# Optimization experiments

Measured on AMD Instinct MI355X. Metric: run time of the kernel, lower is better.

## Reference

```python
import jax, jax.numpy as jnp
import numpy as np

B, C, T = 8, 256, 16000
N_HALF = 32  # d_state // 2 complex modes (S4D stores conjugate pairs)
EPS = 1e-8


def setup_inputs() -> dict:
    key = jax.random.key(0)
    ks = jax.random.split(key, 8)
    x = jax.random.normal(ks[0], (B, C, T), jnp.float32)
    # ChannelwiseLayerNorm params
    gamma = jnp.ones((C,), jnp.float32)
    beta = jnp.zeros((C,), jnp.float32)
    # PReLU per-channel slope (torch default init 0.25)
    prelu_w = jnp.full((C,), 0.25, jnp.float32)
    # S4D kernel params (standard S4D init)
    log_dt = (jax.random.uniform(ks[1], (C,), jnp.float32)
              * (np.log(0.1) - np.log(0.001)) + np.log(0.001)).astype(jnp.float32)
    log_A_real = jnp.log(0.5 * jnp.ones((C, N_HALF), jnp.float32))
    A_imag = jnp.broadcast_to(np.pi * jnp.arange(N_HALF, dtype=jnp.float32), (C, N_HALF))
    C_re = jax.random.normal(ks[2], (C, N_HALF), jnp.float32) * (0.5 ** 0.5)
    C_im = jax.random.normal(ks[3], (C, N_HALF), jnp.float32) * (0.5 ** 0.5)
    D = jax.random.normal(ks[4], (C,), jnp.float32)
    # output 1x1 conv (C -> 2C) followed by GLU over channel dim
    W_out = jax.random.normal(ks[5], (2 * C, C), jnp.float32) * (1.0 / np.sqrt(C))
    b_out = jnp.zeros((2 * C,), jnp.float32)
    return dict(x=x, gamma=gamma, beta=beta, prelu_w=prelu_w, log_dt=log_dt,
                log_A_real=log_A_real, A_imag=A_imag, C_re=C_re, C_im=C_im,
                D=D, W_out=W_out, b_out=b_out)


def reference(x, gamma, beta, prelu_w, log_dt, log_A_real, A_imag, C_re, C_im, D, W_out, b_out):
    # --- channel-wise LayerNorm over C (per timestep), x: [B, C, T] ---
    mean = jnp.mean(x, axis=1, keepdims=True)
    var = jnp.mean((x - mean) ** 2, axis=1, keepdims=True)
    y = (x - mean) * jax.lax.rsqrt(var + EPS)
    y = y * gamma[None, :, None] + beta[None, :, None]
    # --- PReLU (per-channel slope) ---
    y = jnp.where(y >= 0, y, prelu_w[None, :, None] * y)
    # --- S4D convolution kernel via Vandermonde (ZOH discretization) ---
    L = x.shape[-1]
    dt = jnp.exp(log_dt)[:, None]                      # [C, 1]
    A = -jnp.exp(log_A_real) + 1j * A_imag             # [C, N]
    dtA = dt * A                                       # [C, N]
    Cc = (C_re + 1j * C_im) * (jnp.exp(dtA) - 1.0) / A  # [C, N]
    vand = jnp.exp(dtA[:, :, None] * jnp.arange(L))    # [C, N, L]
    k = 2.0 * jnp.real(jnp.einsum('hn,hnl->hl', Cc, vand))  # [C, L]
    # --- FFT-based causal convolution ---
    n = 2 * L
    y_f = jnp.fft.rfft(y, n=n)                         # [B, C, n/2+1]
    k_f = jnp.fft.rfft(k, n=n)                         # [C, n/2+1]
    s = jnp.fft.irfft(y_f * k_f[None], n=n)[..., :L]   # [B, C, T]
    s = s + y * D[None, :, None]                       # skip connection
    # --- GELU + 1x1 conv + GLU over channels ---
    s = jax.nn.gelu(s, approximate=False)
    z = jnp.einsum('bct,oc->bot', s, W_out) + b_out[None, :, None]  # [B, 2C, T]
    out = z[:, :C] * jax.nn.sigmoid(z[:, C:])
    # --- residual ---
    return x + out
```

## Files before the change

kernel.cpp:

```cpp
#include <hip/hip_runtime.h>
#include <cstdint>
#include <cstddef>

constexpr int cB = 8, cC = 256, cT = 16000, cN = 32;
constexpr int cLAM = 128;
constexpr int cP = 125;
constexpr int cPpad = 128;
constexpr float cEPS = 1e-8f;

typedef __bf16 bf16;
typedef __bf16 bf16x4 __attribute__((ext_vector_type(4)));
typedef __bf16 bf16x8 __attribute__((ext_vector_type(8)));
typedef float floatx4 __attribute__((ext_vector_type(4)));

constexpr size_t kMean = 0;
constexpr size_t kRstd = kMean + (size_t)cB * cT * 4;
constexpr size_t kWlr  = kRstd + (size_t)cB * cT * 4;
constexpr size_t kWli  = kWlr + (size_t)cC * cN * 4;
constexpr size_t kWb   = kWli + (size_t)cC * cN * 4;
constexpr size_t kLt   = kWb  + (size_t)512 * 256 * 2;
constexpr size_t kEt   = kLt  + (size_t)cC * 128 * 128 * 2;
constexpr size_t kVt   = kEt  + (size_t)cC * 64 * 128 * 2;
constexpr size_t kU    = kVt  + (size_t)cC * 128 * 64 * 2;

__global__ void prepW_kernel(const float* __restrict__ W_out, bf16* __restrict__ Wb) {
  int idx = blockIdx.x * 256 + threadIdx.x;
  if (idx < 512 * 256) Wb[idx] = (bf16)W_out[idx];
}

__global__ void prep2_kernel(const float* __restrict__ log_dt,
                             const float* __restrict__ log_A_real,
                             const float* __restrict__ A_imag,
                             const float* __restrict__ C_re,
                             const float* __restrict__ C_im,
                             float* __restrict__ wlr, float* __restrict__ wli,
                             bf16* __restrict__ Lt, bf16* __restrict__ Et,
                             bf16* __restrict__ Vt) {
  int c = blockIdx.x;
  int j = threadIdx.x;
  __shared__ float kv[128];
  float dt = expf(log_dt[c]);
  float kj = 0.f;
  for (int n = 0; n < cN; ++n) {
    int idx = c * cN + n;
    float Ar = -expf(log_A_real[idx]);
    float Ai = A_imag[idx];
    float ar = dt * Ar, ai = dt * Ai;
    float mg = expf(ar), cw, sw;
    sincosf(ai, &sw, &cw);
    float wre = mg * cw, wim = mg * sw;
    float den = Ar * Ar + Ai * Ai;
    float emr = wre - 1.f, emi = wim;
    float qr = (emr * Ar + emi * Ai) / den;
    float qi = (emi * Ar - emr * Ai) / den;
    float cre = C_re[idx], cim = C_im[idx];
    float c2r = 2.f * (cre * qr - cim * qi);
    float c2i = 2.f * (cre * qi + cim * qr);
    float mj = expf((float)j * ar), cj, sj;
    sincosf((float)j * ai, &sj, &cj);
    float wjr = mj * cj, wji = mj * sj;
    kj += c2r * wjr - c2i * wji;
    float w1r = wjr * wre - wji * wim;
    float w1i = wjr * wim + wji * wre;
    Vt[(size_t)c * 8192 + j * 64 + 2 * n]     = (bf16)(c2r * w1r - c2i * w1i);
    Vt[(size_t)c * 8192 + j * 64 + 2 * n + 1] = (bf16)(-(c2r * w1i + c2i * w1r));
    float mr = expf((float)(127 - j) * ar), cr2, sr2;
    sincosf((float)(127 - j) * ai, &sr2, &cr2);
    Et[(size_t)c * 8192 + (2 * n) * 128 + j]     = (bf16)(mr * cr2);
    Et[(size_t)c * 8192 + (2 * n + 1) * 128 + j] = (bf16)(mr * sr2);
  }
  kv[j] = kj;
  if (j < cN) {
    int idx = c * cN + j;
    float Ar = -expf(log_A_real[idx]);
    float ai = dt * A_imag[idx], ar = dt * Ar;
    float m = expf(128.f * ar), cc, ss;
    sincosf(128.f * ai, &ss, &cc);
    wlr[idx] = m * cc;
    wli[idx] = m * ss;
  }
  __syncthreads();
  bf16* row = Lt + (size_t)c * 16384 + (size_t)j * 128;
  for (int i = 0; i < 128; i += 4) {
    bf16x4 v;
    for (int q = 0; q < 4; ++q) {
      int ii = i + q;
      v[q] = (ii <= j) ? (bf16)kv[j - ii] : (bf16)0.f;
    }
    *(bf16x4*)(row + i) = v;
  }
}

__global__ void stats_kernel(const float* __restrict__ x,
                             float* __restrict__ meanp, float* __restrict__ rstdp) {
  int g = blockIdx.x * 256 + threadIdx.x;
  int b = g / cT;
  int t = g - b * cT;
  const float* xp = x + (size_t)b * cC * cT + t;
  float s1 = 0.f, s2 = 0.f;
#pragma unroll 8
  for (int c = 0; c < cC; ++c) {
    float v = xp[(size_t)c * cT];
    s1 += v;
    s2 = fmaf(v, v, s2);
  }
  float mean = s1 * (1.0f / cC);
  float var = fmaf(s2, 1.0f / cC, -mean * mean);
  meanp[g] = mean;
  rstdp[g] = rsqrtf(var + cEPS);
}

__global__ __launch_bounds__(256, 2)
void scanM_kernel(const float* __restrict__ x, const float* __restrict__ meanp,
                  const float* __restrict__ rstdp, const float* __restrict__ gam,
                  const float* __restrict__ bet, const float* __restrict__ prw,
                  const float* __restrict__ Dp,
                  const float* __restrict__ wlr, const float* __restrict__ wli,
                  const bf16* __restrict__ Lt, const bf16* __restrict__ Et,
                  const bf16* __restrict__ Vt, bf16* __restrict__ U) {
  __shared__ __align__(16) bf16 Y[128 * 136];
  __shared__ __align__(16) bf16 H[128 * 136];
  __shared__ float Sseg[8][32][2];

  int blk = blockIdx.x;
  int b = blk & 7, c = blk >> 3;
  int tid = threadIdx.x;
  int lane = tid & 63, w = tid >> 6, quad = lane >> 4, mh = lane & 15;
  float gamma = gam[c], beta = bet[c], pw = prw[c], Dc = Dp[c];

  const float4* x4 = (const float4*)(x + (size_t)(b * cC + c) * cT);
  const float4* m4 = (const float4*)(meanp + (size_t)b * cT);
  const float4* r4 = (const float4*)(rstdp + (size_t)b * cT);
#pragma unroll
  for (int it = 0; it < 16; ++it) {
    int i4 = tid + it * 256;
    if (i4 < 4000) {
      float4 xv = x4[i4], mv = m4[i4], rv = r4[i4];
      int t = i4 * 4, p = t >> 7, j = t & 127;
      float ys[4];
      ys[0] = fmaf((xv.x - mv.x) * rv.x, gamma, beta);
      ys[1] = fmaf((xv.y - mv.y) * rv.y, gamma, beta);
      ys[2] = fmaf((xv.z - mv.z) * rv.z, gamma, beta);
      ys[3] = fmaf((xv.w - mv.w) * rv.w, gamma, beta);
      bf16x4 yv;
#pragma unroll
      for (int q = 0; q < 4; ++q) {
        float y = ys[q];
        yv[q] = (bf16)(y >= 0.f ? y : y * pw);
      }
      *(bf16x4*)&Y[p * 136 + j] = yv;
    }
  }
  for (int e = tid; e < 3 * 136; e += 256) Y[125 * 136 + e] = (bf16)0.f;
  __syncthreads();

  const bf16* EtC = Et + (size_t)c * 8192;
  floatx4 hacc[8];
#pragma unroll
  for (int mi = 0; mi < 8; ++mi) hacc[mi] = (floatx4){0.f, 0.f, 0.f, 0.f};
#pragma unroll
  for (int kk = 0; kk < 4; ++kk) {
    bf16x8 bfrag = *(const bf16x8*)(EtC + (w * 16 + mh) * 128 + kk * 32 + quad * 8);
#pragma unroll
    for (int mi = 0; mi < 8; ++mi) {
      bf16x8 af = *(bf16x8*)&Y[(mi * 16 + mh) * 136 + kk * 32 + quad * 8];
      hacc[mi] = __builtin_amdgcn_mfma_f32_16x16x32_bf16(af, bfrag, hacc[mi], 0, 0, 0);
    }
  }
#pragma unroll
  for (int mi = 0; mi < 8; ++mi) {
#pragma unroll
    for (int r = 0; r < 4; ++r) {
      int p = mi * 16 + quad * 4 + r;
      int comp = w * 16 + mh;
      float v = hacc[mi][r];
      bf16 hi = (bf16)v;
      bf16 lo = (bf16)(v - (float)hi);
      H[p * 136 + comp] = hi;
      H[p * 136 + 64 + comp] = lo;
    }
  }
  __syncthreads();

  {
    int n = tid & 31, sg = tid >> 5;
    int p0 = sg * 16;
    int p1 = (p0 + 16 < cP) ? p0 + 16 : cP;
    float wr = wlr[c * cN + n], wi = wli[c * cN + n];
    float hR = 0.f, hI = 0.f;
    for (int p = p0; p < p1; ++p) {
      float sr = (float)H[p * 136 + 2 * n] + (float)H[p * 136 + 64 + 2 * n];
      float si = (float)H[p * 136 + 2 * n + 1] + (float)H[p * 136 + 64 + 2 * n + 1];
      float t1 = fmaf(wr, hR, fmaf(-wi, hI, sr));
      hI = fmaf(wr, hI, fmaf(wi, hR, si));
      hR = t1;
    }
    Sseg[sg][n][0] = hR; Sseg[sg][n][1] = hI;
    __syncthreads();
    if (tid < 32) {
      float ar = wr, ai = wi;
      for (int q = 0; q < 4; ++q) {
        float nr = ar * ar - ai * ai;
        ai = 2.f * ar * ai; ar = nr;
      }
      float HR = 0.f, HI = 0.f;
      for (int s2 = 0; s2 < 8; ++s2) {
        float fr = Sseg[s2][n][0], fi = Sseg[s2][n][1];
        Sseg[s2][n][0] = HR; Sseg[s2][n][1] = HI;
        float t1 = fmaf(ar, HR, fmaf(-ai, HI, fr));
        HI = fmaf(ar, HI, fmaf(ai, HR, fi));
        HR = t1;
      }
    }
    __syncthreads();
    hR = Sseg[sg][n][0]; hI = Sseg[sg][n][1];
    for (int p = p0; p < p1; ++p) {
      float sr = (float)H[p * 136 + 2 * n] + (float)H[p * 136 + 64 + 2 * n];
      float si = (float)H[p * 136 + 2 * n + 1] + (float)H[p * 136 + 64 + 2 * n + 1];
      bf16 hiR = (bf16)hR; bf16 loR = (bf16)(hR - (float)hiR);
      bf16 hiI = (bf16)hI; bf16 loI = (bf16)(hI - (float)hiI);
      H[p * 136 + 2 * n] = hiR;      H[p * 136 + 2 * n + 1] = hiI;
      H[p * 136 + 64 + 2 * n] = loR; H[p * 136 + 64 + 2 * n + 1] = loI;
      float t1 = fmaf(wr, hR, fmaf(-wi, hI, sr));
      hI = fmaf(wr, hI, fmaf(wi, hR, si));
      hR = t1;
    }
  }
  __syncthreads();

  const bf16* LtC = Lt + (size_t)c * 16384;
  const bf16* VtC = Vt + (size_t)c * 8192;
  floatx4 acc[8][2];
#pragma unroll
  for (int mi = 0; mi < 8; ++mi) {
    acc[mi][0] = (floatx4){0.f, 0.f, 0.f, 0.f};
    acc[mi][1] = (floatx4){0.f, 0.f, 0.f, 0.f};
  }
#pragma unroll
  for (int kk = 0; kk < 4; ++kk) {
    bf16x8 b0 = *(const bf16x8*)(LtC + ((2 * w) * 16 + mh) * 128 + kk * 32 + quad * 8);
    bf16x8 b1 = *(const bf16x8*)(LtC + ((2 * w + 1) * 16 + mh) * 128 + kk * 32 + quad * 8);
#pragma unroll
    for (int mi = 0; mi < 8; ++mi) {
      bf16x8 af = *(bf16x8*)&Y[(mi * 16 + mh) * 136 + kk * 32 + quad * 8];
      acc[mi][0] = __builtin_amdgcn_mfma_f32_16x16x32_bf16(af, b0, acc[mi][0], 0, 0, 0);
      acc[mi][1] = __builtin_amdgcn_mfma_f32_16x16x32_bf16(af, b1, acc[mi][1], 0, 0, 0);
    }
  }
#pragma unroll
  for (int kk = 0; kk < 2; ++kk) {
    bf16x8 v0 = *(const bf16x8*)(VtC + ((2 * w) * 16 + mh) * 64 + kk * 32 + quad * 8);
    bf16x8 v1 = *(const bf16x8*)(VtC + ((2 * w + 1) * 16 + mh) * 64 + kk * 32 + quad * 8);
#pragma unroll
    for (int mi = 0; mi < 8; ++mi) {
      bf16x8 ah = *(bf16x8*)&H[(mi * 16 + mh) * 136 + kk * 32 + quad * 8];
      bf16x8 al = *(bf16x8*)&H[(mi * 16 + mh) * 136 + 64 + kk * 32 + quad * 8];
      acc[mi][0] = __builtin_amdgcn_mfma_f32_16x16x32_bf16(ah, v0, acc[mi][0], 0, 0, 0);
      acc[mi][1] = __builtin_amdgcn_mfma_f32_16x16x32_bf16(ah, v1, acc[mi][1], 0, 0, 0);
      acc[mi][0] = __builtin_amdgcn_mfma_f32_16x16x32_bf16(al, v0, acc[mi][0], 0, 0, 0);
      acc[mi][1] = __builtin_amdgcn_mfma_f32_16x16x32_bf16(al, v1, acc[mi][1], 0, 0, 0);
    }
  }
  bf16 ub[8][2][4];
#pragma unroll
  for (int mi = 0; mi < 8; ++mi)
#pragma unroll
    for (int jj = 0; jj < 2; ++jj)
#pragma unroll
      for (int r = 0; r < 4; ++r) {
        int p = mi * 16 + quad * 4 + r;
        int j = (2 * w + jj) * 16 + mh;
        float y = (float)Y[p * 136 + j];
        float sv = fmaf(Dc, y, acc[mi][jj][r]);
        float g = 0.5f * sv * (1.0f + erff(sv * 0.70710678118654752f));
        ub[mi][jj][r] = (bf16)g;
      }
  __syncthreads();
#pragma unroll
  for (int mi = 0; mi < 8; ++mi)
#pragma unroll
    for (int jj = 0; jj < 2; ++jj)
#pragma unroll
      for (int r = 0; r < 4; ++r) {
        int p = mi * 16 + quad * 4 + r;
        int j = (2 * w + jj) * 16 + mh;
        Y[p * 136 + j] = ub[mi][jj][r];
      }
  __syncthreads();
  bf16* Uc = U + (size_t)(b * cC + c) * cT;
#pragma unroll
  for (int it = 0; it < 16; ++it) {
    int i4 = tid + it * 256;
    if (i4 < 4000) {
      int t = i4 * 4, p = t >> 7, j = t & 127;
      *(bf16x4*)(Uc + t) = *(bf16x4*)&Y[p * 136 + j];
    }
  }
}

__global__ __launch_bounds__(256, 2)
void gemm2_kernel(const bf16* __restrict__ U, const bf16* __restrict__ Wb,
                  const float* __restrict__ b_out, const float* __restrict__ x,
                  float* __restrict__ out) {
  __shared__ __align__(16) bf16 Ut[64 * 264];
  int bx = blockIdx.x;
  int tb = bx % 250, b = bx / 250;
  int t0 = tb * 64;
  int tid = threadIdx.x, lane = tid & 63, w = tid >> 6, quad = lane >> 4, mh = lane & 15;
  {
    const bf16* src = U + (size_t)(b * cC + tid) * cT + t0;
#pragma unroll
    for (int g = 0; g < 8; ++g) {
      bf16x8 v = *(const bf16x8*)(src + g * 8);
#pragma unroll
      for (int k = 0; k < 8; ++k) Ut[(g * 8 + k) * 264 + tid] = v[k];
    }
  }
  __syncthreads();
  floatx4 a1[4][4], a2[4][4];
#pragma unroll
  for (int oj = 0; oj < 4; ++oj)
#pragma unroll
    for (int tt = 0; tt < 4; ++tt) {
      a1[oj][tt] = (floatx4){0.f, 0.f, 0.f, 0.f};
      a2[oj][tt] = (floatx4){0.f, 0.f, 0.f, 0.f};
    }
#pragma unroll
  for (int kk = 0; kk < 8; ++kk) {
    int ko = kk * 32 + quad * 8;
    bf16x8 wf1[4], wf2[4];
#pragma unroll
    for (int oj = 0; oj < 4; ++oj) {
      int o = w * 64 + oj * 16 + mh;
      wf1[oj] = *(const bf16x8*)(Wb + (size_t)o * 256 + ko);
      wf2[oj] = *(const bf16x8*)(Wb + (size_t)(o + 256) * 256 + ko);
    }
#pragma unroll
    for (int tt = 0; tt < 4; ++tt) {
      bf16x8 uf = *(bf16x8*)&Ut[(tt * 16 + mh) * 264 + ko];
#pragma unroll
      for (int oj = 0; oj < 4; ++oj) {
        a1[oj][tt] = __builtin_amdgcn_mfma_f32_16x16x32_bf16(wf1[oj], uf, a1[oj][tt], 0, 0, 0);
        a2[oj][tt] = __builtin_amdgcn_mfma_f32_16x16x32_bf16(wf2[oj], uf, a2[oj][tt], 0, 0, 0);
      }
    }
  }
#pragma unroll
  for (int oj = 0; oj < 4; ++oj)
#pragma unroll
    for (int tt = 0; tt < 4; ++tt)
#pragma unroll
      for (int r = 0; r < 4; ++r) {
        int o = w * 64 + oj * 16 + quad * 4 + r;
        int t = t0 + tt * 16 + mh;
        float z1 = a1[oj][tt][r] + b_out[o];
        float z2 = a2[oj][tt][r] + b_out[o + 256];
        float sg = 1.0f / (1.0f + expf(-z2));
        size_t idx = (size_t)(b * cC + o) * cT + t;
        out[idx] = x[idx] + z1 * sg;
      }
}

extern "C" void kernel_launch(void* const* d_in, const int* in_sizes, int n_in,
                              void* d_out, int out_size, void* d_ws, size_t ws_size,
                              hipStream_t stream) {
  const float* x          = (const float*)d_in[0];
  const float* gamma      = (const float*)d_in[1];
  const float* beta       = (const float*)d_in[2];
  const float* prelu_w    = (const float*)d_in[3];
  const float* log_dt     = (const float*)d_in[4];
  const float* log_A_real = (const float*)d_in[5];
  const float* A_imag     = (const float*)d_in[6];
  const float* C_re       = (const float*)d_in[7];
  const float* C_im       = (const float*)d_in[8];
  const float* Dp         = (const float*)d_in[9];
  const float* W_out      = (const float*)d_in[10];
  const float* b_out      = (const float*)d_in[11];
  float* out = (float*)d_out;
  char* ws = (char*)d_ws;

  float* meanp = (float*)(ws + kMean);
  float* rstdp = (float*)(ws + kRstd);
  float* wlr   = (float*)(ws + kWlr);
  float* wli   = (float*)(ws + kWli);
  bf16*  Wb    = (bf16*)(ws + kWb);
  bf16*  Lt    = (bf16*)(ws + kLt);
  bf16*  Et    = (bf16*)(ws + kEt);
  bf16*  Vt    = (bf16*)(ws + kVt);
  bf16*  U     = (bf16*)(ws + kU);

  prepW_kernel<<<512, 256, 0, stream>>>(W_out, Wb);
  prep2_kernel<<<256, 128, 0, stream>>>(log_dt, log_A_real, A_imag, C_re, C_im,
                                        wlr, wli, Lt, Et, Vt);
  stats_kernel<<<(cB * cT) / 256, 256, 0, stream>>>(x, meanp, rstdp);
  scanM_kernel<<<cB * cC, 256, 0, stream>>>(x, meanp, rstdp, gamma, beta, prelu_w,
                                            Dp, wlr, wli, Lt, Et, Vt, U);
  gemm2_kernel<<<cB * (cT / 64), 256, 0, stream>>>(U, Wb, b_out, x, out);
}
```

Baseline: 500.1 us.

## Parallelize stats reduction, split gemm2 outputs, use fast GELU and sigmoid

Restructures the LayerNorm stats kernel so 8 warps each reduce 32 channels and combine through shared memory, which raises parallelism. gemm2 is split into two output-channel halves per time tile with higher occupancy bounds. The exact erf GELU is replaced with the tanh approximation via exp2/rcp intrinsics, and the sigmoid uses fast intrinsics. The Lt Toeplitz write loop is reordered for coalesced stores. The GELU approximation changes numerics slightly, and the gemm2 split reloads the U tile twice.

```diff
diff --git a/kernel.cpp b/kernel.cpp
--- a/kernel.cpp
+++ b/kernel.cpp
@@ -3,9 +3,7 @@
 #include <cstddef>
 
 constexpr int cB = 8, cC = 256, cT = 16000, cN = 32;
-constexpr int cLAM = 128;
 constexpr int cP = 125;
-constexpr int cPpad = 128;
 constexpr float cEPS = 1e-8f;
 
 typedef __bf16 bf16;
@@ -22,6 +20,10 @@
 constexpr size_t kEt   = kLt  + (size_t)cC * 128 * 128 * 2;
 constexpr size_t kVt   = kEt  + (size_t)cC * 64 * 128 * 2;
 constexpr size_t kU    = kVt  + (size_t)cC * 128 * 64 * 2;
+
+__device__ __forceinline__ float fast_sigmoid(float z) {
+  return __builtin_amdgcn_rcpf(1.f + __builtin_amdgcn_exp2f(-z * 1.4426950408889634f));
+}
 
 __global__ void prepW_kernel(const float* __restrict__ W_out, bf16* __restrict__ Wb) {
   int idx = blockIdx.x * 256 + threadIdx.x;
@@ -80,34 +82,48 @@
     wli[idx] = m * ss;
   }
   __syncthreads();
-  bf16* row = Lt + (size_t)c * 16384 + (size_t)j * 128;
-  for (int i = 0; i < 128; i += 4) {
+  bf16* LtC = Lt + (size_t)c * 16384;
+  for (int e = j; e < 4096; e += 128) {
+    int t4 = e * 4;
+    int row = t4 >> 7, col = t4 & 127;
     bf16x4 v;
+#pragma unroll
     for (int q = 0; q < 4; ++q) {
-      int ii = i + q;
-      v[q] = (ii <= j) ? (bf16)kv[j - ii] : (bf16)0.f;
-    }
-    *(bf16x4*)(row + i) = v;
-  }
-}
-
-__global__ void stats_kernel(const float* __restrict__ x,
-                             float* __restrict__ meanp, float* __restrict__ rstdp) {
-  int g = blockIdx.x * 256 + threadIdx.x;
-  int b = g / cT;
-  int t = g - b * cT;
-  const float* xp = x + (size_t)b * cC * cT + t;
+      int ii = col + q;
+      v[q] = (ii <= row) ? (bf16)kv[row - ii] : (bf16)0.f;
+    }
+    *(bf16x4*)(LtC + row * 128 + col) = v;
+  }
+}
+
+__global__ __launch_bounds__(512)
+void stats_kernel(const float* __restrict__ x,
+                  float* __restrict__ meanp, float* __restrict__ rstdp) {
+  __shared__ float r1[8][64], r2[8][64];
+  int g0 = blockIdx.x * 64;
+  int b = g0 / cT;
+  int t0 = g0 - b * cT;
+  int ts = threadIdx.x & 63, cq = threadIdx.x >> 6;
+  const float* xp = x + ((size_t)b * cC + cq * 32) * cT + t0 + ts;
   float s1 = 0.f, s2 = 0.f;
 #pragma unroll 8
-  for (int c = 0; c < cC; ++c) {
+  for (int c = 0; c < 32; ++c) {
     float v = xp[(size_t)c * cT];
     s1 += v;
     s2 = fmaf(v, v, s2);
   }
-  float mean = s1 * (1.0f / cC);
-  float var = fmaf(s2, 1.0f / cC, -mean * mean);
-  meanp[g] = mean;
-  rstdp[g] = rsqrtf(var + cEPS);
+  r1[cq][ts] = s1; r2[cq][ts] = s2;
+  __syncthreads();
+  if (threadIdx.x < 64) {
+    float a1 = 0.f, a2 = 0.f;
+#pragma unroll
+    for (int q = 0; q < 8; ++q) { a1 += r1[q][threadIdx.x]; a2 += r2[q][threadIdx.x]; }
+    float mean = a1 * (1.0f / cC);
+    float var = fmaf(a2, 1.0f / cC, -mean * mean);
+    int g = g0 + threadIdx.x;
+    meanp[g] = mean;
+    rstdp[g] = rsqrtf(var + cEPS);
+  }
 }
 
 __global__ __launch_bounds__(256, 2)
@@ -272,7 +288,11 @@
         int j = (2 * w + jj) * 16 + mh;
         float y = (float)Y[p * 136 + j];
         float sv = fmaf(Dc, y, acc[mi][jj][r]);
-        float g = 0.5f * sv * (1.0f + erff(sv * 0.70710678118654752f));
+        float s3 = sv * sv * sv;
+        float zz = 0.7978845608028654f * fmaf(0.044715f, s3, sv);
+        float e = __builtin_amdgcn_exp2f(zz * 2.8853900817779268f);
+        float th = 1.f - 2.f * __builtin_amdgcn_rcpf(e + 1.f);
+        float g = 0.5f * sv * (1.f + th);
         ub[mi][jj][r] = (bf16)g;
       }
   __syncthreads();
@@ -298,14 +318,17 @@
   }
 }
 
-__global__ __launch_bounds__(256, 2)
+__global__ __launch_bounds__(256, 4)
 void gemm2_kernel(const bf16* __restrict__ U, const bf16* __restrict__ Wb,
                   const float* __restrict__ b_out, const float* __restrict__ x,
                   float* __restrict__ out) {
   __shared__ __align__(16) bf16 Ut[64 * 264];
   int bx = blockIdx.x;
-  int tb = bx % 250, b = bx / 250;
+  int ot = bx & 1;
+  int bt = bx >> 1;
+  int tb = bt % 250, b = bt / 250;
   int t0 = tb * 64;
+  int o0 = ot * 128;
   int tid = threadIdx.x, lane = tid & 63, w = tid >> 6, quad = lane >> 4, mh = lane & 15;
   {
     const bf16* src = U + (size_t)(b * cC + tid) * cT + t0;
@@ -317,9 +340,9 @@
     }
   }
   __syncthreads();
-  floatx4 a1[4][4], a2[4][4];
-#pragma unroll
-  for (int oj = 0; oj < 4; ++oj)
+  floatx4 a1[2][4], a2[2][4];
+#pragma unroll
+  for (int oj = 0; oj < 2; ++oj)
 #pragma unroll
     for (int tt = 0; tt < 4; ++tt) {
       a1[oj][tt] = (floatx4){0.f, 0.f, 0.f, 0.f};
@@ -328,10 +351,10 @@
 #pragma unroll
   for (int kk = 0; kk < 8; ++kk) {
     int ko = kk * 32 + quad * 8;
-    bf16x8 wf1[4], wf2[4];
-#pragma unroll
-    for (int oj = 0; oj < 4; ++oj) {
-      int o = w * 64 + oj * 16 + mh;
+    bf16x8 wf1[2], wf2[2];
+#pragma unroll
+    for (int oj = 0; oj < 2; ++oj) {
+      int o = o0 + w * 32 + oj * 16 + mh;
       wf1[oj] = *(const bf16x8*)(Wb + (size_t)o * 256 + ko);
       wf2[oj] = *(const bf16x8*)(Wb + (size_t)(o + 256) * 256 + ko);
     }
@@ -339,23 +362,23 @@
     for (int tt = 0; tt < 4; ++tt) {
       bf16x8 uf = *(bf16x8*)&Ut[(tt * 16 + mh) * 264 + ko];
 #pragma unroll
-      for (int oj = 0; oj < 4; ++oj) {
+      for (int oj = 0; oj < 2; ++oj) {
         a1[oj][tt] = __builtin_amdgcn_mfma_f32_16x16x32_bf16(wf1[oj], uf, a1[oj][tt], 0, 0, 0);
         a2[oj][tt] = __builtin_amdgcn_mfma_f32_16x16x32_bf16(wf2[oj], uf, a2[oj][tt], 0, 0, 0);
       }
     }
   }
 #pragma unroll
-  for (int oj = 0; oj < 4; ++oj)
+  for (int oj = 0; oj < 2; ++oj)
 #pragma unroll
     for (int tt = 0; tt < 4; ++tt)
 #pragma unroll
       for (int r = 0; r < 4; ++r) {
-        int o = w * 64 + oj * 16 + quad * 4 + r;
+        int o = o0 + w * 32 + oj * 16 + quad * 4 + r;
         int t = t0 + tt * 16 + mh;
         float z1 = a1[oj][tt][r] + b_out[o];
         float z2 = a2[oj][tt][r] + b_out[o + 256];
-        float sg = 1.0f / (1.0f + expf(-z2));
+        float sg = fast_sigmoid(z2);
         size_t idx = (size_t)(b * cC + o) * cT + t;
         out[idx] = x[idx] + z1 * sg;
       }
@@ -392,8 +415,8 @@
   prepW_kernel<<<512, 256, 0, stream>>>(W_out, Wb);
   prep2_kernel<<<256, 128, 0, stream>>>(log_dt, log_A_real, A_imag, C_re, C_im,
                                         wlr, wli, Lt, Et, Vt);
-  stats_kernel<<<(cB * cT) / 256, 256, 0, stream>>>(x, meanp, rstdp);
+  stats_kernel<<<(cB * cT) / 64, 512, 0, stream>>>(x, meanp, rstdp);
   scanM_kernel<<<cB * cC, 256, 0, stream>>>(x, meanp, rstdp, gamma, beta, prelu_w,
                                             Dp, wlr, wli, Lt, Et, Vt, U);
-  gemm2_kernel<<<cB * (cT / 64), 256, 0, stream>>>(U, Wb, b_out, x, out);
-}
+  gemm2_kernel<<<cB * (cT / 64) * 2, 256, 0, stream>>>(U, Wb, b_out, x, out);
+}
```

New measurement: 532.7 us. +6.5%, slower.
